# Kernel tuning notes

Measured on AMD Instinct MI355X. Metric: run time of the kernel, lower is better.

Reference implementation:

```python
import jax, jax.numpy as jnp
import numpy as np

B, FIN, FOUT, FH = 32, 32, 32, 64
H = W = 128
LAT = 512
K_IN, K_MID, K_OUT, K_SHORT = FH * FIN, FH * FH, FOUT * FH, FOUT * FIN
K_TOTAL = K_IN + K_MID + K_OUT + K_SHORT + FH + FH + FOUT + FOUT  # 9408


def setup_inputs() -> dict:
    key = jax.random.key(0)
    ks = jax.random.split(key, 20)
    def rn(k, shape, scale=None):
        s = scale if scale is not None else 1.0 / np.sqrt(shape[-1])
        return jax.random.normal(k, shape, dtype=jnp.float32) * s
    return {
        "x": jax.random.normal(ks[0], (B, FIN, H, W), dtype=jnp.float32),
        "lat": jax.random.normal(ks[1], (B, LAT), dtype=jnp.float32),
        "w0": rn(ks[2], (LAT, LAT)), "b0": rn(ks[3], (LAT,), 0.02),
        "w1a": rn(ks[4], (2 * LAT, LAT)), "b1a": rn(ks[5], (2 * LAT,), 0.02),
        "w1b": rn(ks[6], (LAT, 2 * LAT)), "b1b": rn(ks[7], (LAT,), 0.02),
        "w1s": rn(ks[8], (LAT, LAT)), "b1s": rn(ks[9], (LAT,), 0.02),
        "w2a": rn(ks[10], (2 * LAT, LAT)), "b2a": rn(ks[11], (2 * LAT,), 0.02),
        "w2b": rn(ks[12], (K_TOTAL, 2 * LAT)), "b2b": rn(ks[13], (K_TOTAL,), 0.02),
        "w2s": rn(ks[14], (K_TOTAL, LAT)), "b2s": rn(ks[15], (K_TOTAL,), 0.02),
        "wfa": rn(ks[16], (K_TOTAL, K_TOTAL)), "bfa": rn(ks[17], (K_TOTAL,), 0.02),
    }


def _lrb(h, wa, ba, wb, bb, ws, bs):
    # LinearResidualBlock: shortcut + 2-layer MLP with ReLU
    return h @ ws.T + bs + jax.nn.relu(h @ wa.T + ba) @ wb.T + bb


def reference(x, lat, w0, b0, w1a, b1a, w1b, b1b, w1s, b1s,
              w2a, b2a, w2b, b2b, w2s, b2s, wfa, bfa):
    # hypernetwork: dyna_k then LinearFA (forward is a plain linear)
    h = lat @ w0.T + b0                              # [B, 512]
    h = _lrb(h, w1a, b1a, w1b, b1b, w1s, b1s)        # [B, 512]
    h = _lrb(h, w2a, b2a, w2b, b2b, w2s, b2s)        # [B, K_TOTAL]
    ks = h @ wfa.T + bfa                             # [B, K_TOTAL]

    sizes = [K_IN, K_MID, K_OUT, K_SHORT, FH, FH, FOUT, FOUT]
    offs = np.cumsum([0] + sizes)
    k_in = ks[:, offs[0]:offs[1]].reshape(B, FH, FIN)
    k_mid = ks[:, offs[1]:offs[2]].reshape(B, FH, FH)
    k_out = ks[:, offs[2]:offs[3]].reshape(B, FOUT, FH)
    k_short = ks[:, offs[3]:offs[4]].reshape(B, FOUT, FIN)
    b_in = ks[:, offs[4]:offs[5]][:, :, None, None]    # [B, FH, 1, 1]
    b_mid = ks[:, offs[5]:offs[6]][:, :, None, None]
    b_out = ks[:, offs[6]:offs[7]][:, :, None, None]   # [B, FOUT, 1, 1]
    b_short = ks[:, offs[7]:offs[8]][:, :, None, None]

    # per-sample 1x1 grouped convs == batched matmuls over channels
    xs = jnp.einsum('bihw,boi->bohw', x, k_short) + b_short
    xn = jax.nn.relu(jnp.einsum('bihw,boi->bohw', x, k_in) + b_in)
    xn = jax.nn.relu(jnp.einsum('bihw,boi->bohw', xn, k_mid) + b_mid)
    xn = jnp.einsum('bihw,boi->bohw', xn, k_out) + b_out
    return xn + xs
```

## Files before the change

### kernel.cpp

```cpp
#include <hip/hip_runtime.h>
#include <cstdint>

#define KT 9408
#define NT 256
#define KC 16

__global__ __launch_bounds__(256, 1) void gemm32_partial(
    const float* __restrict__ X1, const float* __restrict__ W1, int K1,
    const float* __restrict__ X2, const float* __restrict__ W2, int K2,
    float* __restrict__ partial, int O, int ksplit)
{
    __shared__ float Xs[KC][32];
    __shared__ float Wt[KC][NT];

    const int t      = threadIdx.x;
    const int o0     = blockIdx.x * NT;
    const int s      = blockIdx.y;
    const int kchunk = (K1 + K2) / ksplit;
    const int kbeg   = s * kchunk;
    const int kend   = kbeg + kchunk;
    const int lane   = t & 63;
    const int wv     = t >> 6;

    const int sr  = t >> 2;
    const int sc4 = (t & 3) << 2;

    float4 wpre[4];
    float  xpre[2];

    {
        int kc0 = kbeg;
#pragma unroll
        for (int p = 0; p < 4; ++p) {
            int r = sr + 64 * p;
            int o = o0 + r;
            int kg = kc0 + sc4;
            float4 v = make_float4(0.f, 0.f, 0.f, 0.f);
            if (o < O)
                v = (kg < K1) ? *(const float4*)&W1[(size_t)o * K1 + kg]
                              : *(const float4*)&W2[(size_t)o * K2 + (kg - K1)];
            wpre[p] = v;
        }
#pragma unroll
        for (int it = 0; it < 2; ++it) {
            int idx = t + 256 * it;
            int kg  = kc0 + (idx >> 5);
            int bb  = idx & 31;
            xpre[it] = (kg < K1) ? X1[(size_t)bb * K1 + kg]
                                 : X2[(size_t)bb * K2 + (kg - K1)];
        }
    }

    float acc[8][4];
#pragma unroll
    for (int bi = 0; bi < 8; bi++)
#pragma unroll
        for (int j = 0; j < 4; j++) acc[bi][j] = 0.f;

    for (int kc0 = kbeg; kc0 < kend; kc0 += KC) {
#pragma unroll
        for (int it = 0; it < 2; ++it) {
            int idx = t + 256 * it;
            Xs[idx >> 5][idx & 31] = xpre[it];
        }
#pragma unroll
        for (int p = 0; p < 4; ++p) {
            int r = sr + 64 * p;
            Wt[sc4 + 0][r] = wpre[p].x;
            Wt[sc4 + 1][r] = wpre[p].y;
            Wt[sc4 + 2][r] = wpre[p].z;
            Wt[sc4 + 3][r] = wpre[p].w;
        }
        __syncthreads();

        if (kc0 + KC < kend) {
            int kn = kc0 + KC;
#pragma unroll
            for (int p = 0; p < 4; ++p) {
                int r = sr + 64 * p;
                int o = o0 + r;
                int kg = kn + sc4;
                float4 v = make_float4(0.f, 0.f, 0.f, 0.f);
                if (o < O)
                    v = (kg < K1) ? *(const float4*)&W1[(size_t)o * K1 + kg]
                                  : *(const float4*)&W2[(size_t)o * K2 + (kg - K1)];
                wpre[p] = v;
            }
#pragma unroll
            for (int it = 0; it < 2; ++it) {
                int idx = t + 256 * it;
                int kg  = kn + (idx >> 5);
                int bb  = idx & 31;
                xpre[it] = (kg < K1) ? X1[(size_t)bb * K1 + kg]
                                     : X2[(size_t)bb * K2 + (kg - K1)];
            }
        }

#pragma unroll
        for (int c = 0; c < KC; c++) {
            float4 xa = *(const float4*)&Xs[c][wv * 8];
            float4 xb = *(const float4*)&Xs[c][wv * 8 + 4];
            float xv[8] = {xa.x, xa.y, xa.z, xa.w, xb.x, xb.y, xb.z, xb.w};
            float w[4];
#pragma unroll
            for (int j = 0; j < 4; j++) w[j] = Wt[c][lane + 64 * j];
#pragma unroll
            for (int bi = 0; bi < 8; bi++)
#pragma unroll
                for (int j = 0; j < 4; j++) acc[bi][j] += xv[bi] * w[j];
        }
        __syncthreads();
    }

#pragma unroll
    for (int bi = 0; bi < 8; bi++) {
        int b = wv * 8 + bi;
#pragma unroll
        for (int j = 0; j < 4; j++) {
            int o = o0 + lane + 64 * j;
            if (o < O)
                partial[((size_t)s * 32 + b) * O + o] = acc[bi][j];
        }
    }
}

__global__ __launch_bounds__(256) void reduce_bias(
    const float* __restrict__ partial, const float* __restrict__ bias1,
    const float* __restrict__ bias2, float* __restrict__ Y, int O, int relu,
    int ksplit)
{
    int idx = blockIdx.x * 256 + threadIdx.x;
    if (idx >= 32 * O) return;
    int b = idx / O, o = idx - b * O;
    float s = bias1[o] + (bias2 ? bias2[o] : 0.f);
    for (int k = 0; k < ksplit; k++)
        s += partial[((size_t)k * 32 + b) * O + o];
    Y[idx] = relu ? fmaxf(s, 0.f) : s;
}

typedef __attribute__((ext_vector_type(8))) short bf16x8;
typedef __attribute__((ext_vector_type(4))) float f32x4;

__device__ inline uint32_t pkbf(float lo, float hi) {
    uint32_t a = __builtin_bit_cast(uint32_t, lo);
    uint32_t b = __builtin_bit_cast(uint32_t, hi);
    a = (a + 0x7FFFu + ((a >> 16) & 1u)) >> 16;
    b = (b + 0x7FFFu + ((b >> 16) & 1u)) & 0xFFFF0000u;
    return a | b;
}
__device__ inline uint32_t pk_hi(float a, float b, float& ra, float& rb) {
    uint32_t ua = __builtin_bit_cast(uint32_t, a);
    uint32_t ub = __builtin_bit_cast(uint32_t, b);
    uint32_t ha = (ua + 0x7FFFu + ((ua >> 16) & 1u)) & 0xFFFF0000u;
    uint32_t hb = (ub + 0x7FFFu + ((ub >> 16) & 1u)) & 0xFFFF0000u;
    ra = a - __builtin_bit_cast(float, ha);
    rb = b - __builtin_bit_cast(float, hb);
    return (ha >> 16) | hb;
}

#define MFMA16(a, b, c) __builtin_amdgcn_mfma_f32_16x16x32_bf16(a, b, c, 0, 0, 0)

__global__ __launch_bounds__(256) void gemm32_mfma(
    const float* __restrict__ X1, const float* __restrict__ W1, int K1,
    const float* __restrict__ X2, const float* __restrict__ W2, int K2,
    float* __restrict__ partial, int O, int ksplit)
{
    const int t  = threadIdx.x;
    const int l  = t & 63;
    const int g  = l >> 4;
    const int n  = l & 15;
    const int o0 = blockIdx.x * 64 + (t >> 6) * 16;
    const int s  = blockIdx.y;
    const int kchunk = (K1 + K2) / ksplit;
    const int kbeg   = s * kchunk;
    const int kend   = kbeg + kchunk;

    f32x4 accA, accB;
#pragma unroll
    for (int r = 0; r < 4; ++r) { accA[r] = 0.f; accB[r] = 0.f; }

#pragma unroll 2
    for (int kc = kbeg; kc < kend; kc += 32) {
        const float* Wr;  const float* Xb;  int kk; int ld;
        if (kc < K1) { Wr = W1; Xb = X1; kk = kc;      ld = K1; }
        else         { Wr = W2; Xb = X2; kk = kc - K1; ld = K2; }

        const float* wp = Wr + (size_t)(o0 + n) * ld + kk + 4 * g;
        float4 wlo = *(const float4*)wp;
        float4 whi = *(const float4*)(wp + 16);
        union { bf16x8 v; uint32_t u[4]; } wf;
        wf.u[0] = pkbf(wlo.x, wlo.y); wf.u[1] = pkbf(wlo.z, wlo.w);
        wf.u[2] = pkbf(whi.x, whi.y); wf.u[3] = pkbf(whi.z, whi.w);

#pragma unroll
        for (int bh = 0; bh < 2; ++bh) {
            const float* xp = Xb + (size_t)(16 * bh + n) * ld + kk + 4 * g;
            float4 xa = *(const float4*)xp;
            float4 xb = *(const float4*)(xp + 16);
            float r0, r1, r2, r3, r4, r5, r6, r7;
            union { bf16x8 v; uint32_t u[4]; } xh, xl;
            xh.u[0] = pk_hi(xa.x, xa.y, r0, r1);
            xh.u[1] = pk_hi(xa.z, xa.w, r2, r3);
            xh.u[2] = pk_hi(xb.x, xb.y, r4, r5);
            xh.u[3] = pk_hi(xb.z, xb.w, r6, r7);
            xl.u[0] = pkbf(r0, r1); xl.u[1] = pkbf(r2, r3);
            xl.u[2] = pkbf(r4, r5); xl.u[3] = pkbf(r6, r7);
            if (bh == 0) {
                accA = MFMA16(xh.v, wf.v, accA);
                accA = MFMA16(xl.v, wf.v, accA);
            } else {
                accB = MFMA16(xh.v, wf.v, accB);
                accB = MFMA16(xl.v, wf.v, accB);
            }
        }
    }

#pragma unroll
    for (int r = 0; r < 4; ++r) {
        partial[((size_t)s * 32 + (4 * g + r)) * O + o0 + n]      = accA[r];
        partial[((size_t)s * 32 + (16 + 4 * g + r)) * O + o0 + n] = accB[r];
    }
}

#define TPW 16

__global__ __launch_bounds__(256, 3) void conv_mfma(
    const float* __restrict__ x, const float* __restrict__ ks,
    float* __restrict__ out)
{
    const int t  = threadIdx.x;
    const int b  = blockIdx.y;
    const int l  = t & 63;
    const int g  = l >> 4;
    const int n  = l & 15;
    const int wid = blockIdx.x * 4 + (t >> 6);

    const float* __restrict__ kb = ks + (size_t)b * KT;
    const float* __restrict__ xbase = x + (size_t)b * 524288 + (size_t)(4 * g) * 16384 + n;
    float* __restrict__ obase = out + (size_t)b * 524288 + (size_t)(4 * g) * 16384 + n;

    float e[8];
    auto loadx = [&](int px0) {
        const float* p = xbase + px0;
        e[0] = p[0]; e[1] = p[16384]; e[2] = p[2 * 16384]; e[3] = p[3 * 16384];
        const float* q = p + (size_t)16 * 16384;
        e[4] = q[0]; e[5] = q[16384]; e[6] = q[2 * 16384]; e[7] = q[3 * 16384];
    };
    loadx(wid * TPW * 16);

    auto loadA = [&](const float* W, int ldw, int row0, int k0) -> bf16x8 {
        const float* p = W + (size_t)(row0 + n) * ldw + k0 + 4 * g;
        float4 lo = *(const float4*)p;
        float4 hi = *(const float4*)(p + 16);
        union { bf16x8 v; uint32_t u[4]; } r;
        r.u[0] = pkbf(lo.x, lo.y);
        r.u[1] = pkbf(lo.z, lo.w);
        r.u[2] = pkbf(hi.x, hi.y);
        r.u[3] = pkbf(hi.z, hi.w);
        return r.v;
    };
    auto loadBias = [&](int off) -> f32x4 {
        float4 v = *(const float4*)&kb[off + 4 * g];
        f32x4 r; r[0] = v.x; r[1] = v.y; r[2] = v.z; r[3] = v.w;
        return r;
    };

    bf16x8 ain[4], amid[4][2], aout[2][2], ashort[2];
#pragma unroll
    for (int rt = 0; rt < 4; ++rt) ain[rt] = loadA(kb, 32, 16 * rt, 0);
#pragma unroll
    for (int ot = 0; ot < 4; ++ot)
#pragma unroll
        for (int kf = 0; kf < 2; ++kf) amid[ot][kf] = loadA(kb + 2048, 64, 16 * ot, 32 * kf);
#pragma unroll
    for (int ot = 0; ot < 2; ++ot)
#pragma unroll
        for (int kf = 0; kf < 2; ++kf) aout[ot][kf] = loadA(kb + 6144, 64, 16 * ot, 32 * kf);
#pragma unroll
    for (int ot = 0; ot < 2; ++ot) ashort[ot] = loadA(kb + 8192, 32, 16 * ot, 0);

    f32x4 bin[4], bmid[4], bos[2];
#pragma unroll
    for (int rt = 0; rt < 4; ++rt) bin[rt] = loadBias(9216 + 16 * rt);
#pragma unroll
    for (int ot = 0; ot < 4; ++ot) bmid[ot] = loadBias(9280 + 16 * ot);
#pragma unroll
    for (int ot = 0; ot < 2; ++ot) {
        f32x4 a = loadBias(9344 + 16 * ot);
        f32x4 c = loadBias(9376 + 16 * ot);
#pragma unroll
        for (int r = 0; r < 4; ++r) a[r] += c[r];
        bos[ot] = a;
    }

#pragma unroll 1
    for (int it = 0; it < TPW; ++it) {
        const int px0 = (wid * TPW + it) * 16;

        union { bf16x8 v; uint32_t u[4]; } bx;
        bx.u[0] = pkbf(e[0], e[1]); bx.u[1] = pkbf(e[2], e[3]);
        bx.u[2] = pkbf(e[4], e[5]); bx.u[3] = pkbf(e[6], e[7]);

        if (it + 1 < TPW) loadx(px0 + 16);

        f32x4 h[4];
#pragma unroll
        for (int rt = 0; rt < 4; ++rt) {
            f32x4 acc = MFMA16(ain[rt], bx.v, bin[rt]);
#pragma unroll
            for (int r = 0; r < 4; ++r) acc[r] = fmaxf(acc[r], 0.f);
            h[rt] = acc;
        }
        union { bf16x8 v; uint32_t u[4]; } hb0, hb1;
        hb0.u[0] = pkbf(h[0][0], h[0][1]); hb0.u[1] = pkbf(h[0][2], h[0][3]);
        hb0.u[2] = pkbf(h[1][0], h[1][1]); hb0.u[3] = pkbf(h[1][2], h[1][3]);
        hb1.u[0] = pkbf(h[2][0], h[2][1]); hb1.u[1] = pkbf(h[2][2], h[2][3]);
        hb1.u[2] = pkbf(h[3][0], h[3][1]); hb1.u[3] = pkbf(h[3][2], h[3][3]);

        f32x4 m[4];
#pragma unroll
        for (int ot = 0; ot < 4; ++ot) {
            f32x4 acc = MFMA16(amid[ot][0], hb0.v, bmid[ot]);
            acc = MFMA16(amid[ot][1], hb1.v, acc);
#pragma unroll
            for (int r = 0; r < 4; ++r) acc[r] = fmaxf(acc[r], 0.f);
            m[ot] = acc;
        }
        union { bf16x8 v; uint32_t u[4]; } mb0, mb1;
        mb0.u[0] = pkbf(m[0][0], m[0][1]); mb0.u[1] = pkbf(m[0][2], m[0][3]);
        mb0.u[2] = pkbf(m[1][0], m[1][1]); mb0.u[3] = pkbf(m[1][2], m[1][3]);
        mb1.u[0] = pkbf(m[2][0], m[2][1]); mb1.u[1] = pkbf(m[2][2], m[2][3]);
        mb1.u[2] = pkbf(m[3][0], m[3][1]); mb1.u[3] = pkbf(m[3][2], m[3][3]);

#pragma unroll
        for (int ot = 0; ot < 2; ++ot) {
            f32x4 acc = MFMA16(ashort[ot], bx.v, bos[ot]);
            acc = MFMA16(aout[ot][0], mb0.v, acc);
            acc = MFMA16(aout[ot][1], mb1.v, acc);
            float* po = obase + (size_t)(16 * ot) * 16384 + px0;
            po[0]         = acc[0];
            po[16384]     = acc[1];
            po[2 * 16384] = acc[2];
            po[3 * 16384] = acc[3];
        }
    }
}

extern "C" void kernel_launch(void* const* d_in, const int* in_sizes, int n_in,
                              void* d_out, int out_size, void* d_ws, size_t ws_size,
                              hipStream_t stream)
{
    const float* x   = (const float*)d_in[0];
    const float* lat = (const float*)d_in[1];
    const float* w0  = (const float*)d_in[2];
    const float* b0  = (const float*)d_in[3];
    const float* w1a = (const float*)d_in[4];
    const float* b1a = (const float*)d_in[5];
    const float* w1b = (const float*)d_in[6];
    const float* b1b = (const float*)d_in[7];
    const float* w1s = (const float*)d_in[8];
    const float* b1s = (const float*)d_in[9];
    const float* w2a = (const float*)d_in[10];
    const float* b2a = (const float*)d_in[11];
    const float* w2b = (const float*)d_in[12];
    const float* b2b = (const float*)d_in[13];
    const float* w2s = (const float*)d_in[14];
    const float* b2s = (const float*)d_in[15];
    const float* wfa = (const float*)d_in[16];
    const float* bfa = (const float*)d_in[17];

    float* ws  = (float*)d_ws;
    float* h0  = ws;
    float* t1  = ws + 16384;
    float* h1  = ws + 49152;
    float* t2  = ws + 65536;
    float* h2  = ws + 98304;
    float* ksb = ws + 399360;
    float* pbuf = (float*)d_out;

    dim3 blk(256);
    auto rg = [](int O) { return dim3((unsigned)((32 * O + 255) / 256)); };

    gemm32_partial<<<dim3(2, 32), blk, 0, stream>>>(lat, w0, 512, nullptr, nullptr, 0, pbuf, 512, 32);
    reduce_bias<<<rg(512), blk, 0, stream>>>(pbuf, b0, nullptr, h0, 512, 0, 32);
    gemm32_partial<<<dim3(4, 32), blk, 0, stream>>>(h0, w1a, 512, nullptr, nullptr, 0, pbuf, 1024, 32);
    reduce_bias<<<rg(1024), blk, 0, stream>>>(pbuf, b1a, nullptr, t1, 1024, 1, 32);
    gemm32_partial<<<dim3(2, 32), blk, 0, stream>>>(h0, w1s, 512, t1, w1b, 1024, pbuf, 512, 32);
    reduce_bias<<<rg(512), blk, 0, stream>>>(pbuf, b1s, b1b, h1, 512, 0, 32);
    gemm32_partial<<<dim3(4, 32), blk, 0, stream>>>(h1, w2a, 512, nullptr, nullptr, 0, pbuf, 1024, 32);
    reduce_bias<<<rg(1024), blk, 0, stream>>>(pbuf, b2a, nullptr, t2, 1024, 1, 32);

    gemm32_mfma<<<dim3(147, 6), blk, 0, stream>>>(h1, w2s, 512, t2, w2b, 1024, pbuf, KT, 6);
    reduce_bias<<<rg(KT), blk, 0, stream>>>(pbuf, b2s, b2b, h2, KT, 0, 6);
    gemm32_mfma<<<dim3(147, 7), blk, 0, stream>>>(h2, wfa, KT, nullptr, nullptr, 0, pbuf, KT, 7);
    reduce_bias<<<rg(KT), blk, 0, stream>>>(pbuf, bfa, nullptr, ksb, KT, 0, 7);

    conv_mfma<<<dim3(16, 32), blk, 0, stream>>>(x, ksb, (float*)d_out);
}
```

Before: 294.3 us.

## Fuse hypernetwork GEMM chain into one persistent kernel with grid barriers

Replaces the twelve separate GEMM and reduce launches of the hypernetwork MLP with a single persistent kernel of 512 blocks. Stages are separated by an atomic-counter grid barrier, and the counter is placed in scratch space inside the output buffer. The small 512/1024-wide layers switch from split-K partial sums plus a separate reduce to per-output dot products reduced in shared memory, with bias and ReLU applied in place. This targets launch overhead and partial-buffer traffic. It relies on all 512 blocks being co-resident, otherwise the barrier can deadlock, and it adds barrier latency between stages.

```diff
diff --git a/kernel.cpp b/kernel.cpp
--- a/kernel.cpp
+++ b/kernel.cpp
@@ -2,141 +2,7 @@
 #include <cstdint>
 
 #define KT 9408
-#define NT 256
-#define KC 16
-
-__global__ __launch_bounds__(256, 1) void gemm32_partial(
-    const float* __restrict__ X1, const float* __restrict__ W1, int K1,
-    const float* __restrict__ X2, const float* __restrict__ W2, int K2,
-    float* __restrict__ partial, int O, int ksplit)
-{
-    __shared__ float Xs[KC][32];
-    __shared__ float Wt[KC][NT];
-
-    const int t      = threadIdx.x;
-    const int o0     = blockIdx.x * NT;
-    const int s      = blockIdx.y;
-    const int kchunk = (K1 + K2) / ksplit;
-    const int kbeg   = s * kchunk;
-    const int kend   = kbeg + kchunk;
-    const int lane   = t & 63;
-    const int wv     = t >> 6;
-
-    const int sr  = t >> 2;
-    const int sc4 = (t & 3) << 2;
-
-    float4 wpre[4];
-    float  xpre[2];
-
-    {
-        int kc0 = kbeg;
-#pragma unroll
-        for (int p = 0; p < 4; ++p) {
-            int r = sr + 64 * p;
-            int o = o0 + r;
-            int kg = kc0 + sc4;
-            float4 v = make_float4(0.f, 0.f, 0.f, 0.f);
-            if (o < O)
-                v = (kg < K1) ? *(const float4*)&W1[(size_t)o * K1 + kg]
-                              : *(const float4*)&W2[(size_t)o * K2 + (kg - K1)];
-            wpre[p] = v;
-        }
-#pragma unroll
-        for (int it = 0; it < 2; ++it) {
-            int idx = t + 256 * it;
-            int kg  = kc0 + (idx >> 5);
-            int bb  = idx & 31;
-            xpre[it] = (kg < K1) ? X1[(size_t)bb * K1 + kg]
-                                 : X2[(size_t)bb * K2 + (kg - K1)];
-        }
-    }
-
-    float acc[8][4];
-#pragma unroll
-    for (int bi = 0; bi < 8; bi++)
-#pragma unroll
-        for (int j = 0; j < 4; j++) acc[bi][j] = 0.f;
-
-    for (int kc0 = kbeg; kc0 < kend; kc0 += KC) {
-#pragma unroll
-        for (int it = 0; it < 2; ++it) {
-            int idx = t + 256 * it;
-            Xs[idx >> 5][idx & 31] = xpre[it];
-        }
-#pragma unroll
-        for (int p = 0; p < 4; ++p) {
-            int r = sr + 64 * p;
-            Wt[sc4 + 0][r] = wpre[p].x;
-            Wt[sc4 + 1][r] = wpre[p].y;
-            Wt[sc4 + 2][r] = wpre[p].z;
-            Wt[sc4 + 3][r] = wpre[p].w;
-        }
-        __syncthreads();
-
-        if (kc0 + KC < kend) {
-            int kn = kc0 + KC;
-#pragma unroll
-            for (int p = 0; p < 4; ++p) {
-                int r = sr + 64 * p;
-                int o = o0 + r;
-                int kg = kn + sc4;
-                float4 v = make_float4(0.f, 0.f, 0.f, 0.f);
-                if (o < O)
-                    v = (kg < K1) ? *(const float4*)&W1[(size_t)o * K1 + kg]
-                                  : *(const float4*)&W2[(size_t)o * K2 + (kg - K1)];
-                wpre[p] = v;
-            }
-#pragma unroll
-            for (int it = 0; it < 2; ++it) {
-                int idx = t + 256 * it;
-                int kg  = kn + (idx >> 5);
-                int bb  = idx & 31;
-                xpre[it] = (kg < K1) ? X1[(size_t)bb * K1 + kg]
-                                     : X2[(size_t)bb * K2 + (kg - K1)];
-            }
-        }
-
-#pragma unroll
-        for (int c = 0; c < KC; c++) {
-            float4 xa = *(const float4*)&Xs[c][wv * 8];
-            float4 xb = *(const float4*)&Xs[c][wv * 8 + 4];
-            float xv[8] = {xa.x, xa.y, xa.z, xa.w, xb.x, xb.y, xb.z, xb.w};
-            float w[4];
-#pragma unroll
-            for (int j = 0; j < 4; j++) w[j] = Wt[c][lane + 64 * j];
-#pragma unroll
-            for (int bi = 0; bi < 8; bi++)
-#pragma unroll
-                for (int j = 0; j < 4; j++) acc[bi][j] += xv[bi] * w[j];
-        }
-        __syncthreads();
-    }
-
-#pragma unroll
-    for (int bi = 0; bi < 8; bi++) {
-        int b = wv * 8 + bi;
-#pragma unroll
-        for (int j = 0; j < 4; j++) {
-            int o = o0 + lane + 64 * j;
-            if (o < O)
-                partial[((size_t)s * 32 + b) * O + o] = acc[bi][j];
-        }
-    }
-}
-
-__global__ __launch_bounds__(256) void reduce_bias(
-    const float* __restrict__ partial, const float* __restrict__ bias1,
-    const float* __restrict__ bias2, float* __restrict__ Y, int O, int relu,
-    int ksplit)
-{
-    int idx = blockIdx.x * 256 + threadIdx.x;
-    if (idx >= 32 * O) return;
-    int b = idx / O, o = idx - b * O;
-    float s = bias1[o] + (bias2 ? bias2[o] : 0.f);
-    for (int k = 0; k < ksplit; k++)
-        s += partial[((size_t)k * 32 + b) * O + o];
-    Y[idx] = relu ? fmaxf(s, 0.f) : s;
-}
+#define NBLK 512
 
 typedef __attribute__((ext_vector_type(8))) short bf16x8;
 typedef __attribute__((ext_vector_type(4))) float f32x4;
@@ -160,17 +26,63 @@
 
 #define MFMA16(a, b, c) __builtin_amdgcn_mfma_f32_16x16x32_bf16(a, b, c, 0, 0, 0)
 
-__global__ __launch_bounds__(256) void gemm32_mfma(
-    const float* __restrict__ X1, const float* __restrict__ W1, int K1,
-    const float* __restrict__ X2, const float* __restrict__ W2, int K2,
-    float* __restrict__ partial, int O, int ksplit)
-{
-    const int t  = threadIdx.x;
+__device__ inline void gbar(int* cnt, int target) {
+    __syncthreads();
+    if (threadIdx.x == 0) {
+        __threadfence();
+        __hip_atomic_fetch_add(cnt, 1, __ATOMIC_ACQ_REL, __HIP_MEMORY_SCOPE_AGENT);
+        while (__hip_atomic_load(cnt, __ATOMIC_ACQUIRE, __HIP_MEMORY_SCOPE_AGENT) < target)
+            __builtin_amdgcn_s_sleep(8);
+        __threadfence();
+    }
+    __syncthreads();
+}
+
+template <int TPC>
+__device__ void small_stage(const float* __restrict__ X1, const float* __restrict__ W1, int K1,
+                            const float* __restrict__ X2, const float* __restrict__ W2, int K2,
+                            const float* __restrict__ bias1, const float* __restrict__ bias2,
+                            float* __restrict__ Y, int O, bool relu,
+                            int blk, int t, float* red)
+{
+    constexpr int CPB = 256 / TPC;
+    const int cl = t / TPC, j = t % TPC;
+    const int c  = blk * CPB + cl;
+    const int o  = c >> 5, b = c & 31;
+    const int K  = K1 + K2;
+    const int iters = K / (TPC * 4);
+
+    float acc = 0.f;
+#pragma unroll 4
+    for (int it = 0; it < iters; ++it) {
+        int kg = it * TPC * 4 + j * 4;
+        const float *xp, *wp;
+        if (kg < K1) { xp = X1 + (size_t)b * K1 + kg;        wp = W1 + (size_t)o * K1 + kg; }
+        else         { xp = X2 + (size_t)b * K2 + (kg - K1); wp = W2 + (size_t)o * K2 + (kg - K1); }
+        float4 xv = *(const float4*)xp;
+        float4 wv = *(const float4*)wp;
+        acc += xv.x * wv.x + xv.y * wv.y + xv.z * wv.z + xv.w * wv.w;
+    }
+    red[t] = acc;
+    __syncthreads();
+    if (j == 0) {
+        float s = bias1[o] + (bias2 ? bias2[o] : 0.f);
+#pragma unroll
+        for (int q = 0; q < TPC; ++q) s += red[cl * TPC + q];
+        Y[(size_t)b * O + o] = relu ? fmaxf(s, 0.f) : s;
+    }
+    __syncthreads();
+}
+
+__device__ void mfma_unit(int u, const float* __restrict__ X1, const float* __restrict__ W1, int K1,
+                          const float* __restrict__ X2, const float* __restrict__ W2, int K2,
+                          float* __restrict__ partial, int O, int ksplit, int t)
+{
     const int l  = t & 63;
     const int g  = l >> 4;
     const int n  = l & 15;
-    const int o0 = blockIdx.x * 64 + (t >> 6) * 16;
-    const int s  = blockIdx.y;
+    const int o0 = (u % 147) * 64 + (t >> 6) * 16;
+    const int s  = u / 147;
     const int kchunk = (K1 + K2) / ksplit;
     const int kbeg   = s * kchunk;
     const int kend   = kbeg + kchunk;
@@ -188,9 +100,9 @@
         const float* wp = Wr + (size_t)(o0 + n) * ld + kk + 4 * g;
         float4 wlo = *(const float4*)wp;
         float4 whi = *(const float4*)(wp + 16);
-        union { bf16x8 v; uint32_t u[4]; } wf;
-        wf.u[0] = pkbf(wlo.x, wlo.y); wf.u[1] = pkbf(wlo.z, wlo.w);
-        wf.u[2] = pkbf(whi.x, whi.y); wf.u[3] = pkbf(whi.z, whi.w);
+        union { bf16x8 v; uint32_t u4[4]; } wf;
+        wf.u4[0] = pkbf(wlo.x, wlo.y); wf.u4[1] = pkbf(wlo.z, wlo.w);
+        wf.u4[2] = pkbf(whi.x, whi.y); wf.u4[3] = pkbf(whi.z, whi.w);
 
 #pragma unroll
         for (int bh = 0; bh < 2; ++bh) {
@@ -198,13 +110,13 @@
             float4 xa = *(const float4*)xp;
             float4 xb = *(const float4*)(xp + 16);
             float r0, r1, r2, r3, r4, r5, r6, r7;
-            union { bf16x8 v; uint32_t u[4]; } xh, xl;
-            xh.u[0] = pk_hi(xa.x, xa.y, r0, r1);
-            xh.u[1] = pk_hi(xa.z, xa.w, r2, r3);
-            xh.u[2] = pk_hi(xb.x, xb.y, r4, r5);
-            xh.u[3] = pk_hi(xb.z, xb.w, r6, r7);
-            xl.u[0] = pkbf(r0, r1); xl.u[1] = pkbf(r2, r3);
-            xl.u[2] = pkbf(r4, r5); xl.u[3] = pkbf(r6, r7);
+            union { bf16x8 v; uint32_t u4[4]; } xh, xl;
+            xh.u4[0] = pk_hi(xa.x, xa.y, r0, r1);
+            xh.u4[1] = pk_hi(xa.z, xa.w, r2, r3);
+            xh.u4[2] = pk_hi(xb.x, xb.y, r4, r5);
+            xh.u4[3] = pk_hi(xb.z, xb.w, r6, r7);
+            xl.u4[0] = pkbf(r0, r1); xl.u4[1] = pkbf(r2, r3);
+            xl.u4[2] = pkbf(r4, r5); xl.u4[3] = pkbf(r6, r7);
             if (bh == 0) {
                 accA = MFMA16(xh.v, wf.v, accA);
                 accA = MFMA16(xl.v, wf.v, accA);
@@ -220,6 +132,55 @@
         partial[((size_t)s * 32 + (4 * g + r)) * O + o0 + n]      = accA[r];
         partial[((size_t)s * 32 + (16 + 4 * g + r)) * O + o0 + n] = accB[r];
     }
+}
+
+__device__ void reduce_stage(const float* __restrict__ partial,
+                             const float* __restrict__ bias1, const float* __restrict__ bias2,
+                             float* __restrict__ Y, int O, int ksplit, int blk, int t)
+{
+    for (int i = blk * 256 + t; i < 32 * O; i += NBLK * 256) {
+        int b = i / O, o = i - b * O;
+        float s = bias1[o] + (bias2 ? bias2[o] : 0.f);
+        for (int k = 0; k < ksplit; ++k)
+            s += partial[((size_t)k * 32 + b) * O + o];
+        Y[i] = s;
+    }
+}
+
+__global__ __launch_bounds__(256, 2) void hyper_fused(
+    const float* __restrict__ lat,
+    const float* __restrict__ w0,  const float* __restrict__ b0,
+    const float* __restrict__ w1a, const float* __restrict__ b1a,
+    const float* __restrict__ w1b, const float* __restrict__ b1b,
+    const float* __restrict__ w1s, const float* __restrict__ b1s,
+    const float* __restrict__ w2a, const float* __restrict__ b2a,
+    const float* __restrict__ w2b, const float* __restrict__ b2b,
+    const float* __restrict__ w2s, const float* __restrict__ b2s,
+    const float* __restrict__ wfa, const float* __restrict__ bfa,
+    float* __restrict__ h0, float* __restrict__ t1, float* __restrict__ h1,
+    float* __restrict__ t2, float* __restrict__ h2, float* __restrict__ ksb,
+    float* __restrict__ pbuf, int* __restrict__ cnt)
+{
+    __shared__ float red[256];
+    const int blk = blockIdx.x, t = threadIdx.x;
+
+    small_stage<8>(lat, w0, 512, nullptr, nullptr, 0, b0, nullptr, h0, 512, false, blk, t, red);
+    gbar(cnt, 1 * NBLK);
+    small_stage<4>(h0, w1a, 512, nullptr, nullptr, 0, b1a, nullptr, t1, 1024, true, blk, t, red);
+    gbar(cnt, 2 * NBLK);
+    small_stage<8>(h0, w1s, 512, t1, w1b, 1024, b1s, b1b, h1, 512, false, blk, t, red);
+    gbar(cnt, 3 * NBLK);
+    small_stage<4>(h1, w2a, 512, nullptr, nullptr, 0, b2a, nullptr, t2, 1024, true, blk, t, red);
+    gbar(cnt, 4 * NBLK);
+    for (int u = blk; u < 147 * 6; u += NBLK)
+        mfma_unit(u, h1, w2s, 512, t2, w2b, 1024, pbuf, KT, 6, t);
+    gbar(cnt, 5 * NBLK);
+    reduce_stage(pbuf, b2s, b2b, h2, KT, 6, blk, t);
+    gbar(cnt, 6 * NBLK);
+    for (int u = blk; u < 147 * 7; u += NBLK)
+        mfma_unit(u, h2, wfa, KT, nullptr, nullptr, 0, pbuf, KT, 7, t);
+    gbar(cnt, 7 * NBLK);
+    reduce_stage(pbuf, bfa, nullptr, ksb, KT, 7, blk, t);
 }
 
 #define TPW 16
@@ -377,23 +338,14 @@
     float* h2  = ws + 98304;
     float* ksb = ws + 399360;
     float* pbuf = (float*)d_out;
-
-    dim3 blk(256);
-    auto rg = [](int O) { return dim3((unsigned)((32 * O + 255) / 256)); };
-
-    gemm32_partial<<<dim3(2, 32), blk, 0, stream>>>(lat, w0, 512, nullptr, nullptr, 0, pbuf, 512, 32);
-    reduce_bias<<<rg(512), blk, 0, stream>>>(pbuf, b0, nullptr, h0, 512, 0, 32);
-    gemm32_partial<<<dim3(4, 32), blk, 0, stream>>>(h0, w1a, 512, nullptr, nullptr, 0, pbuf, 1024, 32);
-    reduce_bias<<<rg(1024), blk, 0, stream>>>(pbuf, b1a, nullptr, t1, 1024, 1, 32);
-    gemm32_partial<<<dim3(2, 32), blk, 0, stream>>>(h0, w1s, 512, t1, w1b, 1024, pbuf, 512, 32);
-    reduce_bias<<<rg(512), blk, 0, stream>>>(pbuf, b1s, b1b, h1, 512, 0, 32);
-    gemm32_partial<<<dim3(4, 32), blk, 0, stream>>>(h1, w2a, 512, nullptr, nullptr, 0, pbuf, 1024, 32);
-    reduce_bias<<<rg(1024), blk, 0, stream>>>(pbuf, b2a, nullptr, t2, 1024, 1, 32);
-
-    gemm32_mfma<<<dim3(147, 6), blk, 0, stream>>>(h1, w2s, 512, t2, w2b, 1024, pbuf, KT, 6);
-    reduce_bias<<<rg(KT), blk, 0, stream>>>(pbuf, b2s, b2b, h2, KT, 0, 6);
-    gemm32_mfma<<<dim3(147, 7), blk, 0, stream>>>(h2, wfa, KT, nullptr, nullptr, 0, pbuf, KT, 7);
-    reduce_bias<<<rg(KT), blk, 0, stream>>>(pbuf, bfa, nullptr, ksb, KT, 0, 7);
-
-    conv_mfma<<<dim3(16, 32), blk, 0, stream>>>(x, ksb, (float*)d_out);
-}
+    int*   cnt  = (int*)((char*)d_out + 62u * 1024u * 1024u);
+
+    hipMemsetAsync(cnt, 0, 4, stream);
+
+    hyper_fused<<<dim3(NBLK), dim3(256), 0, stream>>>(
+        lat, w0, b0, w1a, b1a, w1b, b1b, w1s, b1s,
+        w2a, b2a, w2b, b2b, w2s, b2s, wfa, bfa,
+        h0, t1, h1, t2, h2, ksb, pbuf, cnt);
+
+    conv_mfma<<<dim3(16, 32), dim3(256), 0, stream>>>(x, ksb, (float*)d_out);
+}
```

Result: slower. 740.5 us (+151.6%).
